# Performance work log

Hardware: AMD Instinct MI355X
Metric: run time of the kernel (lower is better)

## Reference

```python
import jax, jax.numpy as jnp
import numpy as np

UNITS = 1536
CHAR_LEN = 256
VOCAB = 80
N_MIX = 10  # mixtures // 3


def lstm_step(x, h, c, W, U, b):
    # Keras LSTM gate order: i, f, g(candidate), o
    z = x @ W + h @ U + b
    i, f, g, o = jnp.split(z, 4, axis=-1)
    c_new = jax.nn.sigmoid(f) * c + jax.nn.sigmoid(i) * jnp.tanh(g)
    h_new = jax.nn.sigmoid(o) * jnp.tanh(c_new)
    return h_new, c_new


def compute_window(sentence, coef, kappa_prev):
    # coef: (1, 30) -> alpha, beta, kappa each (1, 10)
    alpha, beta, kappa = jnp.split(coef, 3, axis=1)
    alpha = jnp.exp(alpha)
    beta = jnp.exp(beta)
    kappa = kappa_prev + jnp.exp(kappa)
    u = jnp.arange(1, CHAR_LEN + 1, dtype=coef.dtype)[:, None]  # (L, 1)
    # (L, 10) -> sum over mixtures -> (L,)
    phi = jnp.sum(alpha * jnp.exp(-beta * (kappa - u) ** 2), axis=1)
    phi = phi.reshape(1, CHAR_LEN)
    w = phi @ sentence  # (1, V)
    last_phi = jnp.sum(alpha * jnp.exp(-beta * (kappa - CHAR_LEN + 1) ** 2), axis=1).reshape(1, 1)
    phi_out = jnp.concatenate([phi, last_phi], axis=-1)  # (1, L+1)
    return w, kappa, phi_out


def setup_inputs() -> dict:
    key = jax.random.key(0)
    ks = jax.random.split(key, 24)
    s = 0.02
    in1 = 3 + VOCAB
    in23 = 3 + VOCAB + UNITS
    return {
        "inputs": jax.random.normal(ks[0], (1, 3), jnp.float32),
        "h1": jax.random.normal(ks[1], (1, UNITS), jnp.float32) * 0.1,
        "c1": jax.random.normal(ks[2], (1, UNITS), jnp.float32) * 0.1,
        "h2": jax.random.normal(ks[3], (1, UNITS), jnp.float32) * 0.1,
        "c2": jax.random.normal(ks[4], (1, UNITS), jnp.float32) * 0.1,
        "h3": jax.random.normal(ks[5], (1, UNITS), jnp.float32) * 0.1,
        "c3": jax.random.normal(ks[6], (1, UNITS), jnp.float32) * 0.1,
        "w_prev": jax.random.uniform(ks[7], (1, VOCAB), jnp.float32),
        "kappa_prev": jax.random.uniform(ks[8], (1, N_MIX), jnp.float32),
        "sentence": jax.random.uniform(ks[9], (CHAR_LEN, VOCAB), jnp.float32),
        "W1": jax.random.normal(ks[10], (in1, 4 * UNITS), jnp.float32) * s,
        "U1": jax.random.normal(ks[11], (UNITS, 4 * UNITS), jnp.float32) * s,
        "b1": jnp.zeros((4 * UNITS,), jnp.float32),
        "Wd": jax.random.normal(ks[12], (UNITS, 30), jnp.float32) * s,
        "bd": jnp.zeros((30,), jnp.float32),
        "W2": jax.random.normal(ks[13], (in23, 4 * UNITS), jnp.float32) * s,
        "U2": jax.random.normal(ks[14], (UNITS, 4 * UNITS), jnp.float32) * s,
        "b2": jnp.zeros((4 * UNITS,), jnp.float32),
        "W3": jax.random.normal(ks[15], (in23, 4 * UNITS), jnp.float32) * s,
        "U3": jax.random.normal(ks[16], (UNITS, 4 * UNITS), jnp.float32) * s,
        "b3": jnp.zeros((4 * UNITS,), jnp.float32),
    }


def reference(inputs, h1, c1, h2, c2, h3, c3, w_prev, kappa_prev, sentence,
              W1, U1, b1, Wd, bd, W2, U2, b2, W3, U3, b3):
    # LSTM 1: input = [strokes, prev window]
    x1 = jnp.concatenate([inputs, w_prev], axis=-1)
    h1n, c1n = lstm_step(x1, h1, c1, W1, U1, b1)
    # Attention window coefficients
    coef = h1n @ Wd + bd  # (1, 30)
    w, kappa, phi = compute_window(sentence, coef, kappa_prev)
    # LSTM 2: input = [strokes, window, lstm1]
    x2 = jnp.concatenate([inputs, w, h1n], axis=-1)
    h2n, c2n = lstm_step(x2, h2, c2, W2, U2, b2)
    # LSTM 3: input = [strokes, window, lstm2]
    x3 = jnp.concatenate([inputs, w, h2n], axis=-1)
    h3n, c3n = lstm_step(x3, h3, c3, W3, U3, b3)
    output = jnp.concatenate([h1n, h2n, h3n], axis=-1)  # (1, 3*units)
    return output
```

## Files before the change

kernel.cpp:

```cpp
#include <hip/hip_runtime.h>
#include <math.h>

#define UNITS 1536
#define COLS  6144
#define VOCAB 80
#define CHAR_LEN 256
#define NMIX 10
#define RCHUNK 32

__device__ __forceinline__ float sigmoidf_(float x) { return 1.0f / (1.0f + __expf(-x)); }

__global__ __launch_bounds__(256)
void gemv_partial(const float* __restrict__ W, const float* __restrict__ U,
                  const float* __restrict__ in3, const float* __restrict__ wv,
                  const float* __restrict__ hW, const float* __restrict__ hU,
                  int rowsW, int rowsTotal,
                  float* __restrict__ partials)
{
    __shared__ float xs[RCHUNK];
    const int t = threadIdx.x;
    const int col = (blockIdx.x * 256 + t) * 4;
    const int r0 = blockIdx.y * RCHUNK;
    const int r1 = min(r0 + RCHUNK, rowsTotal);

    if (t < RCHUNK) {
        const int g = r0 + t;
        float xv = 0.f;
        if (g < rowsTotal) {
            if (g < rowsW) xv = (g < 3) ? in3[g] : ((g < 83) ? wv[g - 3] : hW[g - 83]);
            else           xv = hU[g - rowsW];
        }
        xs[t] = xv;
    }
    __syncthreads();

    float4 acc = make_float4(0.f, 0.f, 0.f, 0.f);
    const int endW = min(r1, rowsW);
    #pragma unroll 4
    for (int g = r0; g < endW; ++g) {
        const float4 v = *reinterpret_cast<const float4*>(W + (size_t)g * COLS + col);
        const float x = xs[g - r0];
        acc.x = fmaf(x, v.x, acc.x); acc.y = fmaf(x, v.y, acc.y);
        acc.z = fmaf(x, v.z, acc.z); acc.w = fmaf(x, v.w, acc.w);
    }
    const int startU = max(r0, rowsW);
    #pragma unroll 4
    for (int g = startU; g < r1; ++g) {
        const float4 v = *reinterpret_cast<const float4*>(U + (size_t)(g - rowsW) * COLS + col);
        const float x = xs[g - r0];
        acc.x = fmaf(x, v.x, acc.x); acc.y = fmaf(x, v.y, acc.y);
        acc.z = fmaf(x, v.z, acc.z); acc.w = fmaf(x, v.w, acc.w);
    }
    *reinterpret_cast<float4*>(partials + (size_t)blockIdx.y * COLS + col) = acc;
}

__global__ __launch_bounds__(1024)
void gate_fused(const float* __restrict__ partials, int nChunks,
                const float* __restrict__ b, const float* __restrict__ c_in,
                float* __restrict__ h_out,
                const float* __restrict__ Wd, float* __restrict__ coefpart)
{
    __shared__ float red[4][4][64];
    __shared__ float zs[4][64];
    __shared__ float hs[64];
    __shared__ float red2[8][30];

    const int t = threadIdx.x;
    const int jj = t & 63;
    const int gate = (t >> 6) & 3;
    const int stripe = t >> 8;
    const int j0 = blockIdx.x * 64;
    const int col = gate * UNITS + j0 + jj;

    float s = 0.f;
    for (int c = stripe; c < nChunks; c += 4)
        s += partials[(size_t)c * COLS + col];
    red[stripe][gate][jj] = s;
    __syncthreads();

    if (t < 256) {
        const float z = b[col] + red[0][gate][jj] + red[1][gate][jj]
                               + red[2][gate][jj] + red[3][gate][jj];
        zs[gate][jj] = z;
    }
    __syncthreads();

    if (t < 64) {
        const float zi = zs[0][t], zf = zs[1][t], zg = zs[2][t], zo = zs[3][t];
        const float cn = sigmoidf_(zf) * c_in[j0 + t] + sigmoidf_(zi) * tanhf(zg);
        const float h = sigmoidf_(zo) * tanhf(cn);
        h_out[j0 + t] = h;
        hs[t] = h;
    }
    __syncthreads();

    if (Wd != nullptr) {
        if (t < 240) {
            const int c30 = t % 30;
            const int rbase = (t / 30) * 8;
            float s2 = 0.f;
            #pragma unroll
            for (int k = 0; k < 8; ++k) {
                const int r = rbase + k;
                s2 = fmaf(hs[r], Wd[(size_t)(j0 + r) * 30 + c30], s2);
            }
            red2[t / 30][c30] = s2;
        }
        __syncthreads();
        if (t < 30) {
            float a = 0.f;
            #pragma unroll
            for (int k = 0; k < 8; ++k) a += red2[k][t];
            coefpart[blockIdx.x * 30 + t] = a;
        }
    }
}

__global__ __launch_bounds__(1024)
void window_b(const float* __restrict__ coefpart, const float* __restrict__ bd,
              const float* __restrict__ kappa_prev, const float* __restrict__ sentence,
              float* __restrict__ w_out)
{
    __shared__ float coef[32];
    __shared__ float al[NMIX], be[NMIX], ka[NMIX];
    __shared__ float phi[CHAR_LEN];
    __shared__ float red[12][VOCAB];

    const int t = threadIdx.x;

    if (t < 30) {
        float s = bd[t];
        #pragma unroll
        for (int bb = 0; bb < 24; ++bb) s += coefpart[bb * 30 + t];
        coef[t] = s;
    }
    __syncthreads();

    if (t < NMIX) {
        al[t] = __expf(coef[t]);
        be[t] = __expf(coef[10 + t]);
        ka[t] = kappa_prev[t] + __expf(coef[20 + t]);
    }
    __syncthreads();

    if (t < CHAR_LEN) {
        const float u = (float)(t + 1);
        float p = 0.f;
        #pragma unroll
        for (int k = 0; k < NMIX; ++k) {
            const float d = ka[k] - u;
            p += al[k] * __expf(-be[k] * d * d);
        }
        phi[t] = p;
    }
    __syncthreads();

    if (t < 960) {
        const int v = t % 80;
        const int stripe = t / 80;
        float s = 0.f;
        for (int u = stripe; u < CHAR_LEN; u += 12)
            s = fmaf(phi[u], sentence[u * VOCAB + v], s);
        red[stripe][v] = s;
    }
    __syncthreads();

    if (t < VOCAB) {
        float s = 0.f;
        #pragma unroll
        for (int k = 0; k < 12; ++k) s += red[k][t];
        w_out[t] = s;
    }
}

extern "C" void kernel_launch(void* const* d_in, const int* in_sizes, int n_in,
                              void* d_out, int out_size, void* d_ws, size_t ws_size,
                              hipStream_t stream) {
    (void)in_sizes; (void)n_in; (void)out_size; (void)ws_size;

    const float* inputs     = (const float*)d_in[0];
    const float* h1         = (const float*)d_in[1];
    const float* c1         = (const float*)d_in[2];
    const float* h2         = (const float*)d_in[3];
    const float* c2         = (const float*)d_in[4];
    const float* h3         = (const float*)d_in[5];
    const float* c3         = (const float*)d_in[6];
    const float* w_prev     = (const float*)d_in[7];
    const float* kappa_prev = (const float*)d_in[8];
    const float* sentence   = (const float*)d_in[9];
    const float* W1 = (const float*)d_in[10];
    const float* U1 = (const float*)d_in[11];
    const float* b1 = (const float*)d_in[12];
    const float* Wd = (const float*)d_in[13];
    const float* bd = (const float*)d_in[14];
    const float* W2 = (const float*)d_in[15];
    const float* U2 = (const float*)d_in[16];
    const float* b2 = (const float*)d_in[17];
    const float* W3 = (const float*)d_in[18];
    const float* U3 = (const float*)d_in[19];
    const float* b3 = (const float*)d_in[20];

    float* out = (float*)d_out;
    float* ws  = (float*)d_ws;
    float* w_vec    = ws;
    float* coefpart = ws + 128;
    float* partials = ws + 1024;

    const int rows1  = 83 + UNITS;
    const int rows23 = 83 + UNITS + UNITS;
    const int ch1  = (rows1  + RCHUNK - 1) / RCHUNK;
    const int ch23 = (rows23 + RCHUNK - 1) / RCHUNK;

    gemv_partial<<<dim3(6, ch1), 256, 0, stream>>>(W1, U1, inputs, w_prev, nullptr, h1,
                                                   83, rows1, partials);
    gate_fused<<<24, 1024, 0, stream>>>(partials, ch1, b1, c1, out, Wd, coefpart);

    window_b<<<1, 1024, 0, stream>>>(coefpart, bd, kappa_prev, sentence, w_vec);

    gemv_partial<<<dim3(6, ch23), 256, 0, stream>>>(W2, U2, inputs, w_vec, out, h2,
                                                    1619, rows23, partials);
    gate_fused<<<24, 1024, 0, stream>>>(partials, ch23, b2, c2, out + UNITS,
                                        nullptr, nullptr);

    gemv_partial<<<dim3(6, ch23), 256, 0, stream>>>(W3, U3, inputs, w_vec, out + UNITS, h3,
                                                    1619, rows23, partials);
    gate_fused<<<24, 1024, 0, stream>>>(partials, ch23, b3, c3, out + 2 * UNITS,
                                        nullptr, nullptr);
}
```

Baseline: 276.0 us.

## Hoist recurrent U-matrix GEMVs of all three LSTMs into one independent launch

```diff
diff --git a/kernel.cpp b/kernel.cpp
--- a/kernel.cpp
+++ b/kernel.cpp
@@ -6,52 +6,87 @@
 #define VOCAB 80
 #define CHAR_LEN 256
 #define NMIX 10
-#define RCHUNK 32
 
 __device__ __forceinline__ float sigmoidf_(float x) { return 1.0f / (1.0f + __expf(-x)); }
 
 __global__ __launch_bounds__(256)
-void gemv_partial(const float* __restrict__ W, const float* __restrict__ U,
-                  const float* __restrict__ in3, const float* __restrict__ wv,
-                  const float* __restrict__ hW, const float* __restrict__ hU,
-                  int rowsW, int rowsTotal,
-                  float* __restrict__ partials)
-{
-    __shared__ float xs[RCHUNK];
-    const int t = threadIdx.x;
+void gemv_indep(const float* __restrict__ W1, const float* __restrict__ U1,
+                const float* __restrict__ U2, const float* __restrict__ U3,
+                const float* __restrict__ W2, const float* __restrict__ W3,
+                const float* __restrict__ in3, const float* __restrict__ wp,
+                const float* __restrict__ h1, const float* __restrict__ h2,
+                const float* __restrict__ h3,
+                float* __restrict__ p1, float* __restrict__ p2, float* __restrict__ p3)
+{
+    __shared__ const float* rps[32];
+    __shared__ float xsh[32];
+    const int t = threadIdx.x;
+    const int cy = blockIdx.y;
+
+    if (t < 32) {
+        const int g = cy * 32 + t;
+        const float* rp = W1;
+        float xv = 0.f;
+        if (g < 83)        { rp = W1 + (size_t)g * COLS;          xv = (g < 3) ? in3[g] : wp[g - 3]; }
+        else if (g < 1619) { rp = U1 + (size_t)(g - 83) * COLS;   xv = h1[g - 83]; }
+        else if (g < 1632) {  }
+        else if (g < 3168) { rp = U2 + (size_t)(g - 1632) * COLS; xv = h2[g - 1632]; }
+        else if (g < 3171) { rp = W2 + (size_t)(g - 3168) * COLS; xv = in3[g - 3168]; }
+        else if (g < 3200) {  }
+        else if (g < 4736) { rp = U3 + (size_t)(g - 3200) * COLS; xv = h3[g - 3200]; }
+        else if (g < 4739) { rp = W3 + (size_t)(g - 4736) * COLS; xv = in3[g - 4736]; }
+        rps[t] = rp; xsh[t] = xv;
+    }
+    __syncthreads();
+
     const int col = (blockIdx.x * 256 + t) * 4;
-    const int r0 = blockIdx.y * RCHUNK;
-    const int r1 = min(r0 + RCHUNK, rowsTotal);
-
-    if (t < RCHUNK) {
-        const int g = r0 + t;
-        float xv = 0.f;
-        if (g < rowsTotal) {
-            if (g < rowsW) xv = (g < 3) ? in3[g] : ((g < 83) ? wv[g - 3] : hW[g - 83]);
-            else           xv = hU[g - rowsW];
-        }
-        xs[t] = xv;
-    }
-    __syncthreads();
-
     float4 acc = make_float4(0.f, 0.f, 0.f, 0.f);
-    const int endW = min(r1, rowsW);
-    #pragma unroll 4
-    for (int g = r0; g < endW; ++g) {
-        const float4 v = *reinterpret_cast<const float4*>(W + (size_t)g * COLS + col);
-        const float x = xs[g - r0];
+    #pragma unroll 8
+    for (int i = 0; i < 32; ++i) {
+        const float4 v = *reinterpret_cast<const float4*>(rps[i] + col);
+        const float x = xsh[i];
         acc.x = fmaf(x, v.x, acc.x); acc.y = fmaf(x, v.y, acc.y);
         acc.z = fmaf(x, v.z, acc.z); acc.w = fmaf(x, v.w, acc.w);
     }
-    const int startU = max(r0, rowsW);
-    #pragma unroll 4
-    for (int g = startU; g < r1; ++g) {
-        const float4 v = *reinterpret_cast<const float4*>(U + (size_t)(g - rowsW) * COLS + col);
-        const float x = xs[g - r0];
+
+    float* zone; int slot;
+    if (cy < 51)       { zone = p1; slot = cy; }
+    else if (cy < 99)  { zone = p2; slot = cy - 51; }
+    else if (cy == 99) { zone = p2; slot = 48; }
+    else if (cy < 148) { zone = p3; slot = cy - 100; }
+    else               { zone = p3; slot = 48; }
+    *reinterpret_cast<float4*>(zone + (size_t)slot * COLS + col) = acc;
+}
+
+__global__ __launch_bounds__(256)
+void gemv_dep(const float* __restrict__ W, const float* __restrict__ wv,
+              const float* __restrict__ hp, float* __restrict__ zoneBase)
+{
+    __shared__ const float* rps[32];
+    __shared__ float xsh[32];
+    const int t = threadIdx.x;
+    const int cy = blockIdx.y;
+
+    if (t < 32) {
+        const int g2 = cy * 32 + t;
+        const float* rp = W + 3 * COLS;
+        float xv = 0.f;
+        if (g2 < 80)        { rp = W + (size_t)(3 + g2) * COLS; xv = wv[g2]; }
+        else if (g2 < 1616) { rp = W + (size_t)(3 + g2) * COLS; xv = hp[g2 - 80]; }
+        rps[t] = rp; xsh[t] = xv;
+    }
+    __syncthreads();
+
+    const int col = (blockIdx.x * 256 + t) * 4;
+    float4 acc = make_float4(0.f, 0.f, 0.f, 0.f);
+    #pragma unroll 8
+    for (int i = 0; i < 32; ++i) {
+        const float4 v = *reinterpret_cast<const float4*>(rps[i] + col);
+        const float x = xsh[i];
         acc.x = fmaf(x, v.x, acc.x); acc.y = fmaf(x, v.y, acc.y);
         acc.z = fmaf(x, v.z, acc.z); acc.w = fmaf(x, v.w, acc.w);
     }
-    *reinterpret_cast<float4*>(partials + (size_t)blockIdx.y * COLS + col) = acc;
+    *reinterpret_cast<float4*>(zoneBase + (size_t)cy * COLS + col) = acc;
 }
 
 __global__ __launch_bounds__(1024)
@@ -204,26 +239,18 @@
     float* ws  = (float*)d_ws;
     float* w_vec    = ws;
     float* coefpart = ws + 128;
-    float* partials = ws + 1024;
-
-    const int rows1  = 83 + UNITS;
-    const int rows23 = 83 + UNITS + UNITS;
-    const int ch1  = (rows1  + RCHUNK - 1) / RCHUNK;
-    const int ch23 = (rows23 + RCHUNK - 1) / RCHUNK;
-
-    gemv_partial<<<dim3(6, ch1), 256, 0, stream>>>(W1, U1, inputs, w_prev, nullptr, h1,
-                                                   83, rows1, partials);
-    gate_fused<<<24, 1024, 0, stream>>>(partials, ch1, b1, c1, out, Wd, coefpart);
-
+    float* pbase    = ws + 1024;
+    float* p1 = pbase;
+    float* p2 = pbase + (size_t)51  * COLS;
+    float* p3 = pbase + (size_t)151 * COLS;
+
+    gemv_indep<<<dim3(6, 149), 256, 0, stream>>>(W1, U1, U2, U3, W2, W3,
+                                                 inputs, w_prev, h1, h2, h3,
+                                                 p1, p2, p3);
+    gate_fused<<<24, 1024, 0, stream>>>(p1, 51, b1, c1, out, Wd, coefpart);
     window_b<<<1, 1024, 0, stream>>>(coefpart, bd, kappa_prev, sentence, w_vec);
-
-    gemv_partial<<<dim3(6, ch23), 256, 0, stream>>>(W2, U2, inputs, w_vec, out, h2,
-                                                    1619, rows23, partials);
-    gate_fused<<<24, 1024, 0, stream>>>(partials, ch23, b2, c2, out + UNITS,
-                                        nullptr, nullptr);
-
-    gemv_partial<<<dim3(6, ch23), 256, 0, stream>>>(W3, U3, inputs, w_vec, out + UNITS, h3,
-                                                    1619, rows23, partials);
-    gate_fused<<<24, 1024, 0, stream>>>(partials, ch23, b3, c3, out + 2 * UNITS,
-                                        nullptr, nullptr);
-}
+    gemv_dep<<<dim3(6, 51), 256, 0, stream>>>(W2, w_vec, out, p2 + (size_t)49 * COLS);
+    gate_fused<<<24, 1024, 0, stream>>>(p2, 100, b2, c2, out + UNITS, nullptr, nullptr);
+    gemv_dep<<<dim3(6, 51), 256, 0, stream>>>(W3, w_vec, out + UNITS, p3 + (size_t)49 * COLS);
+    gate_fused<<<24, 1024, 0, stream>>>(p3, 100, b3, c3, out + 2 * UNITS, nullptr, nullptr);
+}
```

Measured after the change: 275.5 us. No clear change (-0.2%).
